# Optimization experiments

Measured on AMD Instinct MI355X. Metric: run time of the kernel, lower is better.

## Reference

```python
import jax, jax.numpy as jnp
import numpy as np

KSIZE = 3

def setup_inputs() -> dict:
    key = jax.random.key(0)
    k1, k2, k3, k4 = jax.random.split(key, 4)
    B, C, H, W = 4, 64, 256, 512
    x = jax.random.normal(k1, (B, C, H, W), dtype=jnp.float32)
    # precomputed latitude-dependent resampling index into flattened H*W
    idx_flat = jax.random.randint(k2, (KSIZE * H * KSIZE * W,), 0, H * W, dtype=jnp.int64)
    weight = jax.random.normal(k3, (C, C, KSIZE, KSIZE), dtype=jnp.float32) * 0.05
    bias = jax.random.normal(k4, (C,), dtype=jnp.float32) * 0.05
    return {"x": x, "idx_flat": idx_flat, "weight": weight, "bias": bias}

def reference(x, idx_flat, weight, bias):
    B, C, H, W = x.shape
    k = KSIZE
    # latitude-dependent scaled gather: [B, C, H*W] -> [B, C, k*H, k*W]
    x1d = x.reshape(B, C, H * W)
    scaled = jnp.take(x1d, idx_flat, axis=2).reshape(B, C, k * H, k * W)
    # conv with kernel=stride=k, no padding -> [B, C, H, W]
    out = jax.lax.conv_general_dilated(
        scaled, weight,
        window_strides=(k, k), padding='VALID',
        dimension_numbers=('NCHW', 'OIHW', 'NCHW'))
    return out + bias[None, :, None, None]
```

## Files before the change

### kernel.cpp

```cpp
#include <hip/hip_runtime.h>
#include <stdint.h>

#define HW_   131072
#define W_    512
#define C_    64
#define KDIM  576

typedef __bf16 bf16_t;
typedef bf16_t bf16x8 __attribute__((ext_vector_type(8)));
typedef float  f32x4_t __attribute__((ext_vector_type(4)));
typedef float  f32x2_t __attribute__((ext_vector_type(2)));

__device__ __forceinline__ unsigned short f32_to_bf16(float f) {
    union { float f; unsigned u; } v; v.f = f;
    unsigned r = (v.u + 0x7FFFu + ((v.u >> 16) & 1u)) >> 16;
    return (unsigned short)r;
}

__device__ __forceinline__ unsigned pack_bf16(float a, float b) {
    union { unsigned u; __bf16 h[2]; } pk;
    pk.h[0] = (__bf16)a;
    pk.h[1] = (__bf16)b;
    return pk.u;
}

#define XT_BYTES   67108864ull
#define WF_BYTES   73728ull

__global__ __launch_bounds__(256) void k_prep_w(const float* __restrict__ w,
                                                unsigned short* __restrict__ wfrag) {
    int id = blockIdx.x * 256 + threadIdx.x;
    if (id >= 18 * 4 * 64) return;
    int lane = id & 63;
    int nt   = (id >> 6) & 3;
    int kc   = id >> 8;
    int n  = nt * 16 + (lane & 15);
    int k0 = kc * 32 + ((lane >> 4) << 3);
    unsigned short tmp[8];
#pragma unroll
    for (int j = 0; j < 8; ++j) {
        int k = k0 + j;
        int t = k >> 6;
        int c = k & 63;
        tmp[j] = f32_to_bf16(w[(size_t)n * KDIM + c * 9 + t]);
    }
    uint4 v;
    v.x = tmp[0] | ((unsigned)tmp[1] << 16);
    v.y = tmp[2] | ((unsigned)tmp[3] << 16);
    v.z = tmp[4] | ((unsigned)tmp[5] << 16);
    v.w = tmp[6] | ((unsigned)tmp[7] << 16);
    ((uint4*)wfrag)[id] = v;
}

__global__ __launch_bounds__(256) void k_transpose(const float* __restrict__ x,
                                                   unsigned short* __restrict__ xt) {
    __shared__ unsigned short tile[256][66];
    int t    = threadIdx.x;
    int lane = t & 63;
    int wave = t >> 6;
    int gp0 = blockIdx.x * 256;
    int b  = gp0 >> 17;
    int p0 = gp0 & (HW_ - 1);
    const float* xb = x + ((size_t)b * C_) * HW_ + p0;
#pragma unroll
    for (int it = 0; it < 16; ++it) {
        int c0  = (it & 7) * 8 + wave * 2;
        int px0 = ((it >> 3) << 7) + lane * 2;
        const float* s0 = xb + ((size_t)c0 << 17) + px0;
        f32x2_t v0 = __builtin_nontemporal_load((const f32x2_t*)s0);
        f32x2_t v1 = __builtin_nontemporal_load((const f32x2_t*)(s0 + HW_));
        *(unsigned*)&tile[px0 + 0][c0] = pack_bf16(v0.x, v1.x);
        *(unsigned*)&tile[px0 + 1][c0] = pack_bf16(v0.y, v1.y);
    }
    __syncthreads();
    unsigned short* dst = xt + (size_t)gp0 * C_;
#pragma unroll
    for (int it = 0; it < 8; ++it) {
        int cid = it * 256 + t;
        int px  = cid >> 3;
        int ch  = cid & 7;
        uint4 v;
        v.x = *(unsigned*)&tile[px][ch * 8 + 0];
        v.y = *(unsigned*)&tile[px][ch * 8 + 2];
        v.z = *(unsigned*)&tile[px][ch * 8 + 4];
        v.w = *(unsigned*)&tile[px][ch * 8 + 6];
        ((uint4*)(dst + (size_t)px * C_))[ch] = v;
    }
}

__global__ __launch_bounds__(256) void k_gemm(const unsigned short* __restrict__ xt,
                                              const unsigned short* __restrict__ wfrag,
                                              const int* __restrict__ idx,
                                              const float* __restrict__ bias,
                                              float* __restrict__ out) {
    __shared__ unsigned p_lds[128][9];

    int tid  = threadIdx.x;
    int wave = tid >> 6;
    int lane = tid & 63;
    int bid  = blockIdx.x;
    int gbase = (((bid & 7) << 9) + (bid >> 3)) * 128;
    int b = gbase >> 17;

    {
        int px   = tid >> 1;
        int half = tid & 1;
        int g  = gbase + px;
        int hw = g & (HW_ - 1);
        int h = hw >> 9, w = hw & (W_ - 1);
        size_t base = (size_t)(3 * h) * (3 * W_) + 3 * w;
        if (half == 0) {
#pragma unroll
            for (int t = 0; t < 5; ++t)
                p_lds[px][t] = (unsigned)idx[base + (size_t)(t / 3) * (3 * W_) + (t % 3)];
        } else {
#pragma unroll
            for (int t = 5; t < 9; ++t)
                p_lds[px][t] = (unsigned)idx[base + (size_t)(t / 3) * (3 * W_) + (t % 3)];
        }
    }
    __syncthreads();

    int quad = lane >> 4;
    int col  = lane & 15;
    int pxw  = wave * 32;

    unsigned p_reg[9][2];
#pragma unroll
    for (int t = 0; t < 9; ++t) {
        p_reg[t][0] = p_lds[pxw + col][t];
        p_reg[t][1] = p_lds[pxw + 16 + col][t];
    }

    const unsigned short* xtb = xt + (((size_t)b) << 17) * C_;
    const uint4* wf = (const uint4*)wfrag;

    f32x4_t acc[2][4] = {};
    bf16x8 Abuf[3][2];
    bf16x8 Bbuf[3][4];

#define ISSUE(s, slot)                                                              \
    {                                                                               \
        const int t_ = (s) >> 1, h_ = (s) & 1;                                      \
        _Pragma("unroll")                                                           \
        for (int ms = 0; ms < 2; ++ms) {                                            \
            const uint4* ap = (const uint4*)((const char*)xtb +                     \
                ((size_t)p_reg[t_][ms] << 7) + (h_ << 6) + (quad << 4));            \
            Abuf[slot][ms] = __builtin_bit_cast(bf16x8, *ap);                       \
        }                                                                           \
        _Pragma("unroll")                                                           \
        for (int nt = 0; nt < 4; ++nt)                                              \
            Bbuf[slot][nt] = __builtin_bit_cast(bf16x8, wf[((s) * 4 + nt) * 64 + lane]); \
    }

    ISSUE(0, 0)
    ISSUE(1, 1)
    ISSUE(2, 2)
#pragma unroll
    for (int s = 0; s < 18; ++s) {
        const int slot = s % 3;
#pragma unroll
        for (int ms = 0; ms < 2; ++ms)
#pragma unroll
            for (int nt = 0; nt < 4; ++nt)
                acc[ms][nt] = __builtin_amdgcn_mfma_f32_16x16x32_bf16(
                    Abuf[slot][ms], Bbuf[slot][nt], acc[ms][nt], 0, 0, 0);
        if (s + 3 < 18) ISSUE(s + 3, slot)
    }
#undef ISSUE

#pragma unroll
    for (int nt = 0; nt < 4; ++nt) {
        int o = nt * 16 + col;
        float bv = bias[o];
#pragma unroll
        for (int ms = 0; ms < 2; ++ms) {
            int m0 = ms * 16 + quad * 4;
            int hw0 = (gbase + pxw + m0) & (HW_ - 1);
            f32x4_t v = acc[ms][nt];
            v.x += bv; v.y += bv; v.z += bv; v.w += bv;
            __builtin_nontemporal_store(v,
                (f32x4_t*)(out + (((size_t)(b * 64 + o)) << 17) + hw0));
        }
    }
}

__global__ __launch_bounds__(256) void k_fallback(const float* __restrict__ x,
                                                  const int* __restrict__ idx,
                                                  const float* __restrict__ w,
                                                  const float* __restrict__ bias,
                                                  float* __restrict__ out) {
    size_t g = (size_t)blockIdx.x * 256 + threadIdx.x;
    int hw = (int)(g & (HW_ - 1));
    int o  = (int)((g >> 17) & 63);
    int b  = (int)(g >> 23);
    int h = hw >> 9, ww = hw & (W_ - 1);
    size_t ibase = (size_t)(3 * h) * (3 * W_) + 3 * ww;
    int p[9];
#pragma unroll
    for (int th = 0; th < 3; ++th)
#pragma unroll
        for (int tw = 0; tw < 3; ++tw)
            p[th * 3 + tw] = idx[ibase + (size_t)th * (3 * W_) + tw];
    const float* xb = x + (size_t)b * C_ * HW_;
    const float* wo = w + (size_t)o * KDIM;
    float acc = bias[o];
    for (int c = 0; c < C_; ++c) {
        const float* xc = xb + (size_t)c * HW_;
        const float* wc = wo + c * 9;
#pragma unroll
        for (int t = 0; t < 9; ++t)
            acc += xc[p[t]] * wc[t];
    }
    out[g] = acc;
}

extern "C" void kernel_launch(void* const* d_in, const int* in_sizes, int n_in,
                              void* d_out, int out_size, void* d_ws, size_t ws_size,
                              hipStream_t stream) {
    const float* x    = (const float*)d_in[0];
    const int*   idx  = (const int*)d_in[1];
    const float* w    = (const float*)d_in[2];
    const float* bias = (const float*)d_in[3];
    float* out = (float*)d_out;

    if (ws_size >= XT_BYTES + WF_BYTES) {
        unsigned short* xt    = (unsigned short*)d_ws;
        unsigned short* wfrag = (unsigned short*)((char*)d_ws + XT_BYTES);
        k_prep_w   <<<18,   256, 0, stream>>>(w, wfrag);
        k_transpose<<<2048, 256, 0, stream>>>(x, xt);
        k_gemm     <<<4096, 256, 0, stream>>>(xt, wfrag, idx, bias, out);
    } else {
        k_fallback<<<131072, 256, 0, stream>>>(x, idx, w, bias, out);
    }
}
```

Before: 348.2 us.

## Stage weights in LDS and deepen gather pipeline with explicit vmcnt waits

Weight fragments for the first 16 K-steps are copied into 64 KB of LDS per block, and the last two steps are loaded straight into registers. The A-operand gathers go through inline asm global loads with an 8-deep prefetch, ordered by hand-placed s_waitcnt vmcnt. Index loads move from LDS staging to direct per-lane reads, launch bounds request 2 blocks per CU, and output stores drop the nontemporal hint. The goal is to hide the latency of the random gathers and cut repeated global weight reads, at the cost of fragile manual wait counts and LDS pressure that may limit occupancy.

```diff
diff --git a/kernel.cpp b/kernel.cpp
--- a/kernel.cpp
+++ b/kernel.cpp
@@ -10,6 +10,7 @@
 typedef bf16_t bf16x8 __attribute__((ext_vector_type(8)));
 typedef float  f32x4_t __attribute__((ext_vector_type(4)));
 typedef float  f32x2_t __attribute__((ext_vector_type(2)));
+typedef unsigned u32x4 __attribute__((ext_vector_type(4)));
 
 __device__ __forceinline__ unsigned short f32_to_bf16(float f) {
     union { float f; unsigned u; } v; v.f = f;
@@ -88,12 +89,12 @@
     }
 }
 
-__global__ __launch_bounds__(256) void k_gemm(const unsigned short* __restrict__ xt,
-                                              const unsigned short* __restrict__ wfrag,
-                                              const int* __restrict__ idx,
-                                              const float* __restrict__ bias,
-                                              float* __restrict__ out) {
-    __shared__ unsigned p_lds[128][9];
+__global__ __launch_bounds__(256, 2) void k_gemm(const unsigned short* __restrict__ xt,
+                                                 const unsigned short* __restrict__ wfrag,
+                                                 const int* __restrict__ idx,
+                                                 const float* __restrict__ bias,
+                                                 float* __restrict__ out) {
+    __shared__ u32x4 blds[4096];
 
     int tid  = threadIdx.x;
     int wave = tid >> 6;
@@ -102,72 +103,101 @@
     int gbase = (((bid & 7) << 9) + (bid >> 3)) * 128;
     int b = gbase >> 17;
 
-    {
-        int px   = tid >> 1;
-        int half = tid & 1;
-        int g  = gbase + px;
-        int hw = g & (HW_ - 1);
-        int h = hw >> 9, w = hw & (W_ - 1);
-        size_t base = (size_t)(3 * h) * (3 * W_) + 3 * w;
-        if (half == 0) {
-#pragma unroll
-            for (int t = 0; t < 5; ++t)
-                p_lds[px][t] = (unsigned)idx[base + (size_t)(t / 3) * (3 * W_) + (t % 3)];
-        } else {
-#pragma unroll
-            for (int t = 5; t < 9; ++t)
-                p_lds[px][t] = (unsigned)idx[base + (size_t)(t / 3) * (3 * W_) + (t % 3)];
-        }
-    }
-    __syncthreads();
-
     int quad = lane >> 4;
     int col  = lane & 15;
     int pxw  = wave * 32;
 
+    {
+        const u32x4* wfv = (const u32x4*)wfrag;
+#pragma unroll
+        for (int i = 0; i < 16; ++i)
+            blds[i * 256 + tid] = wfv[i * 256 + tid];
+    }
+
     unsigned p_reg[9][2];
 #pragma unroll
-    for (int t = 0; t < 9; ++t) {
-        p_reg[t][0] = p_lds[pxw + col][t];
-        p_reg[t][1] = p_lds[pxw + 16 + col][t];
-    }
+    for (int ms = 0; ms < 2; ++ms) {
+        int g  = gbase + pxw + ms * 16 + col;
+        int hw = g & (HW_ - 1);
+        int h = hw >> 9, w = hw & (W_ - 1);
+        const int* ib = idx + (size_t)(3 * h) * (3 * W_) + 3 * w;
+#pragma unroll
+        for (int t = 0; t < 9; ++t)
+            p_reg[t][ms] = (unsigned)ib[(t / 3) * (3 * W_) + (t % 3)];
+    }
+
+    __syncthreads();
 
     const unsigned short* xtb = xt + (((size_t)b) << 17) * C_;
-    const uint4* wf = (const uint4*)wfrag;
 
     f32x4_t acc[2][4] = {};
-    bf16x8 Abuf[3][2];
-    bf16x8 Bbuf[3][4];
-
-#define ISSUE(s, slot)                                                              \
-    {                                                                               \
-        const int t_ = (s) >> 1, h_ = (s) & 1;                                      \
-        _Pragma("unroll")                                                           \
-        for (int ms = 0; ms < 2; ++ms) {                                            \
-            const uint4* ap = (const uint4*)((const char*)xtb +                     \
-                ((size_t)p_reg[t_][ms] << 7) + (h_ << 6) + (quad << 4));            \
-            Abuf[slot][ms] = __builtin_bit_cast(bf16x8, *ap);                       \
-        }                                                                           \
-        _Pragma("unroll")                                                           \
-        for (int nt = 0; nt < 4; ++nt)                                              \
-            Bbuf[slot][nt] = __builtin_bit_cast(bf16x8, wf[((s) * 4 + nt) * 64 + lane]); \
-    }
-
-    ISSUE(0, 0)
-    ISSUE(1, 1)
-    ISSUE(2, 2)
-#pragma unroll
-    for (int s = 0; s < 18; ++s) {
-        const int slot = s % 3;
-#pragma unroll
-        for (int ms = 0; ms < 2; ++ms)
-#pragma unroll
-            for (int nt = 0; nt < 4; ++nt)
-                acc[ms][nt] = __builtin_amdgcn_mfma_f32_16x16x32_bf16(
-                    Abuf[slot][ms], Bbuf[slot][nt], acc[ms][nt], 0, 0, 0);
-        if (s + 3 < 18) ISSUE(s + 3, slot)
-    }
-#undef ISSUE
+    u32x4 Abuf[8][2];
+    u32x4 Bp[2][4];
+    u32x4 Bt[2][4];
+
+#define GLOADX4(dst, addr)                                                       \
+    asm volatile("global_load_dwordx4 %0, %1, off"                               \
+                 : "=&v"(dst) : "v"((const void*)(addr)) : "memory")
+#define WAITVM(n)                                                                \
+    { asm volatile("s_waitcnt vmcnt(" #n ")" ::: "memory");                      \
+      __builtin_amdgcn_sched_barrier(0); }
+#define ISSUE_A(s)                                                               \
+    { const int t_ = (s) >> 1, h_ = (s) & 1;                                     \
+      GLOADX4(Abuf[(s) & 7][0], (const char*)xtb +                               \
+              (((size_t)p_reg[t_][0] << 7) + (h_ << 6) + (quad << 4)));          \
+      GLOADX4(Abuf[(s) & 7][1], (const char*)xtb +                               \
+              (((size_t)p_reg[t_][1] << 7) + (h_ << 6) + (quad << 4))); }
+#define READ_B(s)                                                                \
+    { _Pragma("unroll")                                                          \
+      for (int nt = 0; nt < 4; ++nt)                                             \
+          Bp[(s) & 1][nt] = blds[((s) * 4 + nt) * 64 + lane]; }
+#define MFMA8(s, BSRC)                                                           \
+    { _Pragma("unroll")                                                          \
+      for (int ms = 0; ms < 2; ++ms)                                             \
+      _Pragma("unroll")                                                          \
+      for (int nt = 0; nt < 4; ++nt)                                             \
+          acc[ms][nt] = __builtin_amdgcn_mfma_f32_16x16x32_bf16(                 \
+              __builtin_bit_cast(bf16x8, Abuf[(s) & 7][ms]),                     \
+              __builtin_bit_cast(bf16x8, (BSRC)[nt]), acc[ms][nt], 0, 0, 0); }
+
+    {
+        const char* wfb = (const char*)wfrag;
+#pragma unroll
+        for (int nt = 0; nt < 4; ++nt)
+            GLOADX4(Bt[0][nt], wfb + (size_t)((16 * 4 + nt) * 64 + lane) * 16);
+#pragma unroll
+        for (int nt = 0; nt < 4; ++nt)
+            GLOADX4(Bt[1][nt], wfb + (size_t)((17 * 4 + nt) * 64 + lane) * 16);
+    }
+    ISSUE_A(0) ISSUE_A(1) ISSUE_A(2) ISSUE_A(3)
+    ISSUE_A(4) ISSUE_A(5) ISSUE_A(6) ISSUE_A(7)
+
+    READ_B(0)
+
+    WAITVM(14) READ_B(1)  MFMA8(0,  Bp[0]) ISSUE_A(8)
+    WAITVM(14) READ_B(2)  MFMA8(1,  Bp[1]) ISSUE_A(9)
+    WAITVM(14) READ_B(3)  MFMA8(2,  Bp[0]) ISSUE_A(10)
+    WAITVM(14) READ_B(4)  MFMA8(3,  Bp[1]) ISSUE_A(11)
+    WAITVM(14) READ_B(5)  MFMA8(4,  Bp[0]) ISSUE_A(12)
+    WAITVM(14) READ_B(6)  MFMA8(5,  Bp[1]) ISSUE_A(13)
+    WAITVM(14) READ_B(7)  MFMA8(6,  Bp[0]) ISSUE_A(14)
+    WAITVM(14) READ_B(8)  MFMA8(7,  Bp[1]) ISSUE_A(15)
+    WAITVM(14) READ_B(9)  MFMA8(8,  Bp[0]) ISSUE_A(16)
+    WAITVM(14) READ_B(10) MFMA8(9,  Bp[1]) ISSUE_A(17)
+    WAITVM(14) READ_B(11) MFMA8(10, Bp[0])
+    WAITVM(12) READ_B(12) MFMA8(11, Bp[1])
+    WAITVM(10) READ_B(13) MFMA8(12, Bp[0])
+    WAITVM(8)  READ_B(14) MFMA8(13, Bp[1])
+    WAITVM(6)  READ_B(15) MFMA8(14, Bp[0])
+    WAITVM(4)             MFMA8(15, Bp[1])
+    WAITVM(2)             MFMA8(16, Bt[0])
+    WAITVM(0)             MFMA8(17, Bt[1])
+
+#undef GLOADX4
+#undef WAITVM
+#undef ISSUE_A
+#undef READ_B
+#undef MFMA8
 
 #pragma unroll
     for (int nt = 0; nt < 4; ++nt) {
@@ -179,8 +209,7 @@
             int hw0 = (gbase + pxw + m0) & (HW_ - 1);
             f32x4_t v = acc[ms][nt];
             v.x += bv; v.y += bv; v.z += bv; v.w += bv;
-            __builtin_nontemporal_store(v,
-                (f32x4_t*)(out + (((size_t)(b * 64 + o)) << 17) + hw0));
+            *(f32x4_t*)(out + (((size_t)(b * 64 + o)) << 17) + hw0) = v;
         }
     }
 }
```

Result: faster. 329.8 us (-5.3%).
